# Kernel optimization log

Measured on AMD Instinct MI355X. Metric: run time of the kernel, lower is better.

The kernel has to match this reference:

```python
import jax, jax.numpy as jnp
import numpy as np

N, E = 50000, 800000
IN, HID, H, C = 128, 64, 4, 2
NEG_SLOPE = 0.2


def _gat_layer(h, src, dst, W, al, ar, b, out_dim, residual, resW=None, act='elu'):
    # h: [N, in]; W: [H*out, in]; al/ar: [H, out]; b: [H*out]
    n = h.shape[0]
    feat = (h @ W.T).reshape(n, H, out_dim)            # [N, H, out]
    el = jnp.einsum('nho,ho->nh', feat, al)            # [N, H]
    er = jnp.einsum('nho,ho->nh', feat, ar)            # [N, H]
    e = jax.nn.leaky_relu(el[src] + er[dst], NEG_SLOPE)  # [E, H]
    # segment softmax over incoming edges of each dst node
    emax = jax.ops.segment_max(e, dst, num_segments=n)
    ee = jnp.exp(e - emax[dst])
    denom = jax.ops.segment_sum(ee, dst, num_segments=n)
    alpha = ee / denom[dst]                             # [E, H]
    msg = feat[src] * alpha[:, :, None]                 # [E, H, out]
    rst = jax.ops.segment_sum(msg, dst, num_segments=n)  # [N, H, out]
    if residual == 'id':
        rst = rst + h.reshape(n, H, out_dim)
    elif residual == 'fc':
        rst = rst + (h @ resW.T).reshape(n, H, out_dim)
    rst = rst + b.reshape(1, H, out_dim)
    if act == 'elu':
        rst = jax.nn.elu(rst)
    else:  # softmax over last dim (F.softmax)
        rst = jax.nn.softmax(rst, axis=-1)
    return rst


def setup_inputs() -> dict:
    key = jax.random.key(0)
    ks = jax.random.split(key, 24)
    x = jax.random.normal(ks[0], (N, IN), dtype=jnp.float32)
    src = jax.random.randint(ks[1], (E,), 0, N)
    dst = jax.random.randint(ks[2], (E,), 0, N)
    s = 0.1
    d = {'x': x, 'src': src, 'dst': dst}
    # layer 1: IN -> (H, HID), no residual
    d['W1'] = jax.random.normal(ks[3], (H * HID, IN), dtype=jnp.float32) * s
    d['al1'] = jax.random.normal(ks[4], (H, HID), dtype=jnp.float32) * s
    d['ar1'] = jax.random.normal(ks[5], (H, HID), dtype=jnp.float32) * s
    d['b1'] = jnp.zeros((H * HID,), dtype=jnp.float32)
    # layers 2,3: H*HID -> (H, HID), identity residual
    d['W2'] = jax.random.normal(ks[6], (H * HID, H * HID), dtype=jnp.float32) * s
    d['al2'] = jax.random.normal(ks[7], (H, HID), dtype=jnp.float32) * s
    d['ar2'] = jax.random.normal(ks[8], (H, HID), dtype=jnp.float32) * s
    d['b2'] = jnp.zeros((H * HID,), dtype=jnp.float32)
    d['W3'] = jax.random.normal(ks[9], (H * HID, H * HID), dtype=jnp.float32) * s
    d['al3'] = jax.random.normal(ks[10], (H, HID), dtype=jnp.float32) * s
    d['ar3'] = jax.random.normal(ks[11], (H, HID), dtype=jnp.float32) * s
    d['b3'] = jnp.zeros((H * HID,), dtype=jnp.float32)
    # layer 4: H*HID -> (H, C), linear residual, softmax activation, mean over heads
    d['W4'] = jax.random.normal(ks[12], (H * C, H * HID), dtype=jnp.float32) * s
    d['al4'] = jax.random.normal(ks[13], (H, C), dtype=jnp.float32) * s
    d['ar4'] = jax.random.normal(ks[14], (H, C), dtype=jnp.float32) * s
    d['b4'] = jnp.zeros((H * C,), dtype=jnp.float32)
    d['resW4'] = jax.random.normal(ks[15], (H * C, H * HID), dtype=jnp.float32) * s
    return d


def reference(x, src, dst, W1, al1, ar1, b1, W2, al2, ar2, b2, W3, al3, ar3, b3, W4, al4, ar4, b4, resW4):
    h = _gat_layer(x, src, dst, W1, al1, ar1, b1, HID, 'none', act='elu').reshape(N, H * HID)
    h = _gat_layer(h, src, dst, W2, al2, ar2, b2, HID, 'id', act='elu').reshape(N, H * HID)
    h = _gat_layer(h, src, dst, W3, al3, ar3, b3, HID, 'id', act='elu').reshape(N, H * HID)
    h = _gat_layer(h, src, dst, W4, al4, ar4, b4, C, 'fc', resW=resW4, act='softmax')
    return h.mean(axis=1)  # [N, C]
```

## Files before the change

kernel.cpp:

```cpp
#include <hip/hip_runtime.h>
#include <hip/hip_bf16.h>
#include <math.h>


#define LEAKY_SLOPE 0.2f

typedef __bf16 bf16x8_t __attribute__((ext_vector_type(8)));
typedef float f32x4_t __attribute__((ext_vector_type(4)));
typedef float f32x2_t __attribute__((ext_vector_type(2)));

__device__ __forceinline__ float leaky(float x) { return x > 0.f ? x : LEAKY_SLOPE * x; }
__device__ __forceinline__ float eluf(float x)  { return x > 0.f ? x : expm1f(x); }
__device__ __forceinline__ float bflo(unsigned u) { return __uint_as_float(u << 16); }
__device__ __forceinline__ float bfhi(unsigned u) { return __uint_as_float(u & 0xffff0000u); }
__device__ __forceinline__ unsigned pk2(float a, float b) {
  __hip_bfloat162 t;
  t.x = __float2bfloat16(a);
  t.y = __float2bfloat16(b);
  return *(unsigned*)&t;
}

__device__ __forceinline__ float rlf(float v, int l) {
  return __uint_as_float((unsigned)__builtin_amdgcn_readlane((int)__float_as_uint(v), l));
}
template <int CTRL>
__device__ __forceinline__ float dpp_add(float x) {
  int t = __builtin_amdgcn_update_dpp(0, (int)__float_as_uint(x), CTRL, 0xf, 0xf, false);
  return x + __uint_as_float((unsigned)t);
}
__device__ __forceinline__ float wsum_dpp(float x) {
  x = dpp_add<0x111>(x);
  x = dpp_add<0x112>(x);
  x = dpp_add<0x114>(x);
  x = dpp_add<0x118>(x);
  x = dpp_add<0x142>(x);
  x = dpp_add<0x143>(x);
  return rlf(x, 63);
}
__device__ __forceinline__ float rowsum_dpp(float x) {
  x = dpp_add<0x111>(x);
  x = dpp_add<0x112>(x);
  x = dpp_add<0x114>(x);
  x = dpp_add<0x118>(x);
  return x;
}
__device__ __forceinline__ float wmax(float v) {
#pragma unroll
  for (int o = 32; o; o >>= 1) v = fmaxf(v, __shfl_xor(v, o));
  return v;
}
__device__ __forceinline__ float wsum_sh(float v) {
#pragma unroll
  for (int o = 32; o; o >>= 1) v += __shfl_xor(v, o);
  return v;
}

__device__ __forceinline__ void quad_fma(f32x2_t& a0, f32x2_t& a1, f32x2_t& a2, f32x2_t& a3,
                                         uint4 u, float w) {
  f32x2_t wv = {w, w};
  f32x2_t f;
  f[0] = bflo(u.x); f[1] = bfhi(u.x); a0 = __builtin_elementwise_fma(wv, f, a0);
  f[0] = bflo(u.y); f[1] = bfhi(u.y); a1 = __builtin_elementwise_fma(wv, f, a1);
  f[0] = bflo(u.z); f[1] = bfhi(u.z); a2 = __builtin_elementwise_fma(wv, f, a2);
  f[0] = bflo(u.w); f[1] = bfhi(u.w); a3 = __builtin_elementwise_fma(wv, f, a3);
}

__device__ __forceinline__ void gl_lds16(const __hip_bfloat16* g, __bf16* l) {
  __builtin_amdgcn_global_load_lds((const __attribute__((address_space(1))) void*)g,
                                   (__attribute__((address_space(3))) void*)l, 16, 0, 0);
}

__global__ __launch_bounds__(1024) void scan1_k(const int* __restrict__ deg,
                                                int* __restrict__ rowp,
                                                int* __restrict__ bsum, int n) {
  __shared__ int wtot[16];
  __shared__ int wpre[16];
  int tid = threadIdx.x, lane = tid & 63, wid = tid >> 6;
  int i = blockIdx.x * 1024 + tid;
  int v = (i < n) ? deg[i] : 0;
  int x = v;
#pragma unroll
  for (int off = 1; off < 64; off <<= 1) {
    int t = __shfl_up(x, off);
    if (lane >= off) x += t;
  }
  if (lane == 63) wtot[wid] = x;
  __syncthreads();
  if (wid == 0 && lane < 16) {
    int s = wtot[lane];
    int y = s;
#pragma unroll
    for (int off = 1; off < 16; off <<= 1) {
      int t = __shfl_up(y, off);
      if (lane >= off) y += t;
    }
    wpre[lane] = y - s;
    if (lane == 15) bsum[blockIdx.x] = y;
  }
  __syncthreads();
  if (i < n) rowp[i] = wpre[wid] + x - v;
}

__global__ void scan23_k(const int* __restrict__ bsum, int* __restrict__ rowp, int n, int nb) {
  __shared__ int pref[65];
  int tid = threadIdx.x;
  if (tid < 64) {
    int v = (tid < nb) ? bsum[tid] : 0;
    int x = v;
#pragma unroll
    for (int off = 1; off < 64; off <<= 1) {
      int t = __shfl_up(x, off);
      if (tid >= off) x += t;
    }
    pref[tid] = x - v;
    if (tid == 63) pref[64] = x;
  }
  __syncthreads();
  int i = blockIdx.x * 256 + tid;
  if (i < n) rowp[i] += pref[i >> 10];
  if (i == n) rowp[n] = pref[64];
}

__global__ void scatter_k(const int* __restrict__ src, const int* __restrict__ dst,
                          const int* __restrict__ rowp, const int* __restrict__ slot,
                          int* __restrict__ csrc, int e) {
  int i = blockIdx.x * 256 + threadIdx.x;
  if (i < e) csrc[rowp[dst[i]] + slot[i]] = src[i];
}

__global__ void cvthist_k(const float* __restrict__ W1, const float* __restrict__ W2,
                          const float* __restrict__ W3, const float* __restrict__ W4,
                          const float* __restrict__ rW4,
                          __hip_bfloat16* __restrict__ W1b, __hip_bfloat16* __restrict__ W2b,
                          __hip_bfloat16* __restrict__ W3b, __hip_bfloat16* __restrict__ Wcatb,
                          const int* __restrict__ dst, int* __restrict__ deg,
                          int* __restrict__ slot, int e) {
  int i = blockIdx.x * 256 + threadIdx.x;
  if (i < e) {
    int p = atomicAdd(&deg[dst[i]], 1);
    slot[i] = p;
  }
  if (i < 41984) {
    const float* sp;
    __hip_bfloat16* dp;
    int idx;
    if (i < 8192)       { sp = W1;  dp = W1b;          idx = i; }
    else if (i < 24576) { sp = W2;  dp = W2b;          idx = i - 8192; }
    else if (i < 40960) { sp = W3;  dp = W3b;          idx = i - 24576; }
    else if (i < 41472) { sp = W4;  dp = Wcatb;        idx = i - 40960; }
    else                { sp = rW4; dp = Wcatb + 2048; idx = i - 41472; }
    float4 wv = ((const float4*)sp)[idx];
    uint2 o = {pk2(wv.x, wv.y), pk2(wv.z, wv.w)};
    ((uint2*)dp)[idx] = o;
  }
}

__global__ __launch_bounds__(256) void gemm1f_mfma(const float* __restrict__ A,
                                                   const __hip_bfloat16* __restrict__ B,
                                                   __hip_bfloat16* __restrict__ featb,
                                                   const float* __restrict__ al,
                                                   const float* __restrict__ ar,
                                                   float* __restrict__ el,
                                                   float* __restrict__ er, int n, int nbx) {
  __shared__ __bf16 As[2][128 * 32];
  __shared__ __bf16 Bs[2][128 * 32];
  const int wg = blockIdx.x;
  const int b = ((wg >> 4) << 3) + (wg & 7);
  if (b >= nbx) return;
  const int cb = (wg >> 3) & 1;
  const int r0 = b * 128, c0 = cb * 128;

  const int tid = threadIdx.x;
  const int lane = tid & 63, w = tid >> 6;
  const int tm = lane & 15, tq = lane >> 4;
  const int wm = (w & 1) * 64, wn = (w >> 1) * 64;

  f32x4_t acc[4][4];
#pragma unroll
  for (int i = 0; i < 4; ++i)
#pragma unroll
    for (int j = 0; j < 4; ++j) acc[i][j] = 0.f;

  const int srow = tid >> 1;
  const int sh = tid & 1;
  const int arw = r0 + srow;
  const bool aok = arw < n;
  const float* ap = A + (size_t)arw * 128 + sh * 32;

  const int srB = w * 32 + (lane >> 2);
  const int scB = (lane & 3) * 8;
  const __hip_bfloat16* gb0 = B + (size_t)(c0 + srB) * 128 + scB;

#pragma unroll
  for (int kk = 0; kk < 128; kk += 64) {
    float4 av0 = {0, 0, 0, 0}, av1 = {0, 0, 0, 0}, av2 = {0, 0, 0, 0}, av3 = {0, 0, 0, 0};
    float4 av4 = {0, 0, 0, 0}, av5 = {0, 0, 0, 0}, av6 = {0, 0, 0, 0}, av7 = {0, 0, 0, 0};
    if (aok) {
      const float4* p = (const float4*)(ap + kk);
      av0 = p[0]; av1 = p[1]; av2 = p[2]; av3 = p[3];
      av4 = p[4]; av5 = p[5]; av6 = p[6]; av7 = p[7];
    }
    __syncthreads();
    const __hip_bfloat16* gbk = gb0 + kk;
    gl_lds16(gbk, &Bs[0][w * 1024]);
    gl_lds16(gbk + (size_t)16 * 128, &Bs[0][w * 1024 + 512]);
    gl_lds16(gbk + 32, &Bs[1][w * 1024]);
    gl_lds16(gbk + (size_t)16 * 128 + 32, &Bs[1][w * 1024 + 512]);
    {
      uint4 o;
      o.x = pk2(av0.x, av0.y); o.y = pk2(av0.z, av0.w);
      o.z = pk2(av1.x, av1.y); o.w = pk2(av1.z, av1.w);
      *(uint4*)&As[sh][srow * 32 + 0] = o;
      o.x = pk2(av2.x, av2.y); o.y = pk2(av2.z, av2.w);
      o.z = pk2(av3.x, av3.y); o.w = pk2(av3.z, av3.w);
      *(uint4*)&As[sh][srow * 32 + 8] = o;
      o.x = pk2(av4.x, av4.y); o.y = pk2(av4.z, av4.w);
      o.z = pk2(av5.x, av5.y); o.w = pk2(av5.z, av5.w);
      *(uint4*)&As[sh][srow * 32 + 16] = o;
      o.x = pk2(av6.x, av6.y); o.y = pk2(av6.z, av6.w);
      o.z = pk2(av7.x, av7.y); o.w = pk2(av7.z, av7.w);
      *(uint4*)&As[sh][srow * 32 + 24] = o;
    }
    __syncthreads();
#pragma unroll
    for (int ks = 0; ks < 2; ++ks) {
      bf16x8_t af[4], bfr[4];
#pragma unroll
      for (int i = 0; i < 4; ++i)
        af[i] = *(const bf16x8_t*)&As[ks][(wm + i * 16 + tm) * 32 + tq * 8];
#pragma unroll
      for (int j = 0; j < 4; ++j)
        bfr[j] = *(const bf16x8_t*)&Bs[ks][(wn + j * 16 + tm) * 32 + tq * 8];
#pragma unroll
      for (int i = 0; i < 4; ++i)
#pragma unroll
        for (int j = 0; j < 4; ++j)
          acc[i][j] = __builtin_amdgcn_mfma_f32_16x16x32_bf16(af[i], bfr[j], acc[i][j], 0, 0, 0);
    }
  }

#pragma unroll
  for (int i = 0; i < 4; ++i) {
#pragma unroll
    for (int j = 0; j < 4; ++j) {
      int col = c0 + wn + j * 16 + tm;
#pragma unroll
      for (int rr = 0; rr < 4; ++rr) {
        int row = r0 + wm + i * 16 + tq * 4 + rr;
        if (row < n) featb[(size_t)row * 256 + col] = __float2bfloat16(acc[i][j][rr]);
      }
    }
  }

  {
    const int hd = (c0 + wn) >> 6;
    float alv[4], arv[4];
#pragma unroll
    for (int j = 0; j < 4; ++j) {
      alv[j] = al[hd * 64 + j * 16 + tm];
      arv[j] = ar[hd * 64 + j * 16 + tm];
    }
#pragma unroll
    for (int i = 0; i < 4; ++i) {
#pragma unroll
      for (int rr = 0; rr < 4; ++rr) {
        float se = acc[i][0][rr] * alv[0] + acc[i][1][rr] * alv[1] +
                   acc[i][2][rr] * alv[2] + acc[i][3][rr] * alv[3];
        float sr2 = acc[i][0][rr] * arv[0] + acc[i][1][rr] * arv[1] +
                    acc[i][2][rr] * arv[2] + acc[i][3][rr] * arv[3];
        se = rowsum_dpp(se);
        sr2 = rowsum_dpp(sr2);
        if (tm == 15) {
          int row = r0 + wm + i * 16 + tq * 4 + rr;
          if (row < n) {
            el[(size_t)row * 4 + hd] = se;
            er[(size_t)row * 4 + hd] = sr2;
          }
        }
      }
    }
  }
}

template <int K>
__global__ __launch_bounds__(256) void gemm_mfma(const __hip_bfloat16* __restrict__ A,
                                                 const __hip_bfloat16* __restrict__ B,
                                                 __hip_bfloat16* __restrict__ featb,
                                                 const float* __restrict__ al,
                                                 const float* __restrict__ ar,
                                                 float* __restrict__ el,
                                                 float* __restrict__ er, int n, int nbx) {
  __shared__ __bf16 As[2][128 * 32];
  __shared__ __bf16 Bs[2][128 * 32];
  const int wg = blockIdx.x;
  const int b = ((wg >> 4) << 3) + (wg & 7);
  if (b >= nbx) return;
  const int cb = (wg >> 3) & 1;
  const int r0 = b * 128, c0 = cb * 128;

  const int tid = threadIdx.x;
  const int lane = tid & 63, w = tid >> 6;
  const int tm = lane & 15, tq = lane >> 4;
  const int wm = (w & 1) * 64, wn = (w >> 1) * 64;

  f32x4_t acc[4][4];
#pragma unroll
  for (int i = 0; i < 4; ++i)
#pragma unroll
    for (int j = 0; j < 4; ++j) acc[i][j] = 0.f;

  const bool interior = (r0 + 128 <= n);
  if (interior) {
    const int srow = w * 32 + (lane >> 2);
    const int scol = (lane & 3) * 8;
    const __hip_bfloat16* ga0 = A + (size_t)(r0 + srow) * K + scol;
    const __hip_bfloat16* gb0 = B + (size_t)(c0 + srow) * K + scol;
    for (int kk = 0; kk < K; kk += 64) {
      const __hip_bfloat16* ga = ga0 + kk;
      const __hip_bfloat16* gb = gb0 + kk;
      __syncthreads();
      gl_lds16(ga, &As[0][w * 1024]);
      gl_lds16(ga + (size_t)16 * K, &As[0][w * 1024 + 512]);
      gl_lds16(ga + 32, &As[1][w * 1024]);
      gl_lds16(ga + (size_t)16 * K + 32, &As[1][w * 1024 + 512]);
      gl_lds16(gb, &Bs[0][w * 1024]);
      gl_lds16(gb + (size_t)16 * K, &Bs[0][w * 1024 + 512]);
      gl_lds16(gb + 32, &Bs[1][w * 1024]);
      gl_lds16(gb + (size_t)16 * K + 32, &Bs[1][w * 1024 + 512]);
      __syncthreads();
#pragma unroll
      for (int ks = 0; ks < 2; ++ks) {
        bf16x8_t af[4], bfr[4];
#pragma unroll
        for (int i = 0; i < 4; ++i)
          af[i] = *(const bf16x8_t*)&As[ks][(wm + i * 16 + tm) * 32 + tq * 8];
#pragma unroll
        for (int j = 0; j < 4; ++j)
          bfr[j] = *(const bf16x8_t*)&Bs[ks][(wn + j * 16 + tm) * 32 + tq * 8];
#pragma unroll
        for (int i = 0; i < 4; ++i)
#pragma unroll
          for (int j = 0; j < 4; ++j)
            acc[i][j] = __builtin_amdgcn_mfma_f32_16x16x32_bf16(af[i], bfr[j], acc[i][j], 0, 0, 0);
      }
    }
  } else {
    const int srow = tid >> 1, sko = (tid & 1) * 16;
    for (int kk = 0; kk < K; kk += 32) {
      uint4 av0 = {0, 0, 0, 0}, av1 = {0, 0, 0, 0};
      int arw = r0 + srow;
      if (arw < n) {
        const uint4* p = (const uint4*)(A + (size_t)arw * K + kk + sko);
        av0 = p[0];
        av1 = p[1];
      }
      const uint4* q = (const uint4*)(B + (size_t)(c0 + srow) * K + kk + sko);
      uint4 bv0 = q[0], bv1 = q[1];
      __syncthreads();
      *(uint4*)&As[0][srow * 32 + sko] = av0;
      *(uint4*)&As[0][srow * 32 + sko + 8] = av1;
      *(uint4*)&Bs[0][srow * 32 + sko] = bv0;
      *(uint4*)&Bs[0][srow * 32 + sko + 8] = bv1;
      __syncthreads();
      bf16x8_t af[4], bfr[4];
#pragma unroll
      for (int i = 0; i < 4; ++i)
        af[i] = *(const bf16x8_t*)&As[0][(wm + i * 16 + tm) * 32 + tq * 8];
#pragma unroll
      for (int j = 0; j < 4; ++j)
        bfr[j] = *(const bf16x8_t*)&Bs[0][(wn + j * 16 + tm) * 32 + tq * 8];
#pragma unroll
      for (int i = 0; i < 4; ++i)
#pragma unroll
        for (int j = 0; j < 4; ++j)
          acc[i][j] = __builtin_amdgcn_mfma_f32_16x16x32_bf16(af[i], bfr[j], acc[i][j], 0, 0, 0);
    }
  }

#pragma unroll
  for (int i = 0; i < 4; ++i) {
#pragma unroll
    for (int j = 0; j < 4; ++j) {
      int col = c0 + wn + j * 16 + tm;
#pragma unroll
      for (int rr = 0; rr < 4; ++rr) {
        int row = r0 + wm + i * 16 + tq * 4 + rr;
        if (row < n) featb[(size_t)row * 256 + col] = __float2bfloat16(acc[i][j][rr]);
      }
    }
  }

  {
    const int hd = (c0 + wn) >> 6;
    float alv[4], arv[4];
#pragma unroll
    for (int j = 0; j < 4; ++j) {
      alv[j] = al[hd * 64 + j * 16 + tm];
      arv[j] = ar[hd * 64 + j * 16 + tm];
    }
#pragma unroll
    for (int i = 0; i < 4; ++i) {
#pragma unroll
      for (int rr = 0; rr < 4; ++rr) {
        float se = acc[i][0][rr] * alv[0] + acc[i][1][rr] * alv[1] +
                   acc[i][2][rr] * alv[2] + acc[i][3][rr] * alv[3];
        float sr2 = acc[i][0][rr] * arv[0] + acc[i][1][rr] * arv[1] +
                    acc[i][2][rr] * arv[2] + acc[i][3][rr] * arv[3];
        se = rowsum_dpp(se);
        sr2 = rowsum_dpp(sr2);
        if (tm == 15) {
          int row = r0 + wm + i * 16 + tq * 4 + rr;
          if (row < n) {
            el[(size_t)row * 4 + hd] = se;
            er[(size_t)row * 4 + hd] = sr2;
          }
        }
      }
    }
  }
}

template <int RES>
__global__ __launch_bounds__(256) void agg64_k(const __hip_bfloat16* __restrict__ featb,
                                               const float* __restrict__ el,
                                               const float* __restrict__ er,
                                               const int* __restrict__ rowp,
                                               const int* __restrict__ csrc,
                                               const __hip_bfloat16* __restrict__ hinb,
                                               const float* __restrict__ bias,
                                               __hip_bfloat16* __restrict__ houtb, int n) {
  __shared__ float wsh[4][256];
  __shared__ int ssh[4][64];
  int wv = threadIdx.x >> 6;
  int node = blockIdx.x * 4 + wv;
  int lane = threadIdx.x & 63;
  if (node >= n) return;
  int s0 = rowp[node], s1 = rowp[node + 1];
  int deg = s1 - s0;
  float4 erv = *(const float4*)(er + (size_t)node * 4);

  if (deg <= 64) {
    int sown = 0;
    float x0 = 0.f, x1 = 0.f, x2 = 0.f, x3 = 0.f;
    if (lane < deg) {
      sown = csrc[s0 + lane];
      float4 e = *(const float4*)(el + (size_t)sown * 4);
      x0 = __expf(leaky(e.x + erv.x));
      x1 = __expf(leaky(e.y + erv.y));
      x2 = __expf(leaky(e.z + erv.z));
      x3 = __expf(leaky(e.w + erv.w));
    }
    float d0 = wsum_dpp(x0), d1 = wsum_dpp(x1), d2 = wsum_dpp(x2), d3 = wsum_dpp(x3);
    float i0 = d0 > 0.f ? 1.f / d0 : 0.f;
    float i1 = d1 > 0.f ? 1.f / d1 : 0.f;
    float i2 = d2 > 0.f ? 1.f / d2 : 0.f;
    float i3 = d3 > 0.f ? 1.f / d3 : 0.f;
    float4 wq = {x0 * i0, x1 * i1, x2 * i2, x3 * i3};
    *(float4*)&wsh[wv][lane * 4] = wq;
    ssh[wv][lane] = sown;

    const int half = lane >> 5, sub = lane & 31;
    const int hh = sub >> 3;
    f32x2_t a0 = {0.f, 0.f}, a1 = {0.f, 0.f}, a2 = {0.f, 0.f}, a3 = {0.f, 0.f};
    const int G = deg >> 3;
    int k = 0;
    if (G) {
      int ke = half;
      int sk0 = ssh[wv][ke], sk1 = ssh[wv][ke + 2];
      int sk2 = ssh[wv][ke + 4], sk3 = ssh[wv][ke + 6];
      uint4 u0 = ((const uint4*)(featb + ((size_t)sk0 << 8)))[sub];
      uint4 u1 = ((const uint4*)(featb + ((size_t)sk1 << 8)))[sub];
      uint4 u2 = ((const uint4*)(featb + ((size_t)sk2 << 8)))[sub];
      uint4 u3 = ((const uint4*)(featb + ((size_t)sk3 << 8)))[sub];
      float w0 = wsh[wv][ke * 4 + hh];
      float w1 = wsh[wv][(ke + 2) * 4 + hh];
      float w2 = wsh[wv][(ke + 4) * 4 + hh];
      float w3 = wsh[wv][(ke + 6) * 4 + hh];
      for (int g = 1; g < G; ++g) {
        int kb = g * 8 + half;
        int t0 = ssh[wv][kb], t1 = ssh[wv][kb + 2];
        int t2 = ssh[wv][kb + 4], t3 = ssh[wv][kb + 6];
        uint4 v0 = ((const uint4*)(featb + ((size_t)t0 << 8)))[sub];
        uint4 v1 = ((const uint4*)(featb + ((size_t)t1 << 8)))[sub];
        uint4 v2 = ((const uint4*)(featb + ((size_t)t2 << 8)))[sub];
        uint4 v3 = ((const uint4*)(featb + ((size_t)t3 << 8)))[sub];
        float y0 = wsh[wv][kb * 4 + hh];
        float y1 = wsh[wv][(kb + 2) * 4 + hh];
        float y2 = wsh[wv][(kb + 4) * 4 + hh];
        float y3 = wsh[wv][(kb + 6) * 4 + hh];
        quad_fma(a0, a1, a2, a3, u0, w0);
        quad_fma(a0, a1, a2, a3, u1, w1);
        quad_fma(a0, a1, a2, a3, u2, w2);
        quad_fma(a0, a1, a2, a3, u3, w3);
        u0 = v0; u1 = v1; u2 = v2; u3 = v3;
        w0 = y0; w1 = y1; w2 = y2; w3 = y3;
      }
      quad_fma(a0, a1, a2, a3, u0, w0);
      quad_fma(a0, a1, a2, a3, u1, w1);
      quad_fma(a0, a1, a2, a3, u2, w2);
      quad_fma(a0, a1, a2, a3, u3, w3);
      k = G * 8;
    }
    for (; k < deg; k += 2) {
      int ke = k + half;
      int sk = ssh[wv][ke];
      uint4 u = ((const uint4*)(featb + ((size_t)sk << 8)))[sub];
      float wk = wsh[wv][ke * 4 + hh];
      quad_fma(a0, a1, a2, a3, u, wk);
    }
    a0[0] += __shfl_xor(a0[0], 32); a0[1] += __shfl_xor(a0[1], 32);
    a1[0] += __shfl_xor(a1[0], 32); a1[1] += __shfl_xor(a1[1], 32);
    a2[0] += __shfl_xor(a2[0], 32); a2[1] += __shfl_xor(a2[1], 32);
    a3[0] += __shfl_xor(a3[0], 32); a3[1] += __shfl_xor(a3[1], 32);

    if (half == 0) {
      size_t base = (size_t)node * 256 + sub * 8;
      float v0 = a0[0], v1 = a0[1], v2 = a1[0], v3 = a1[1];
      float v4 = a2[0], v5 = a2[1], v6 = a3[0], v7 = a3[1];
      float4 b0 = *(const float4*)(bias + sub * 8);
      float4 b1 = *(const float4*)(bias + sub * 8 + 4);
      v0 += b0.x; v1 += b0.y; v2 += b0.z; v3 += b0.w;
      v4 += b1.x; v5 += b1.y; v6 += b1.z; v7 += b1.w;
      if (RES) {
        uint4 r = *(const uint4*)(hinb + base);
        v0 += bflo(r.x); v1 += bfhi(r.x);
        v2 += bflo(r.y); v3 += bfhi(r.y);
        v4 += bflo(r.z); v5 += bfhi(r.z);
        v6 += bflo(r.w); v7 += bfhi(r.w);
      }
      uint4 o;
      o.x = pk2(eluf(v0), eluf(v1));
      o.y = pk2(eluf(v2), eluf(v3));
      o.z = pk2(eluf(v4), eluf(v5));
      o.w = pk2(eluf(v6), eluf(v7));
      *(uint4*)(houtb + base) = o;
    }
  } else {
    int hsel = lane >> 4;
    f32x2_t a01 = {0.f, 0.f}, a23 = {0.f, 0.f};
    float m0 = -INFINITY, m1 = -INFINITY, m2 = -INFINITY, m3 = -INFINITY;
    for (int k = s0 + lane; k < s1; k += 64) {
      int s = csrc[k];
      float4 e = *(const float4*)(el + (size_t)s * 4);
      m0 = fmaxf(m0, leaky(e.x + erv.x));
      m1 = fmaxf(m1, leaky(e.y + erv.y));
      m2 = fmaxf(m2, leaky(e.z + erv.z));
      m3 = fmaxf(m3, leaky(e.w + erv.w));
    }
    m0 = wmax(m0); m1 = wmax(m1); m2 = wmax(m2); m3 = wmax(m3);
    float d0 = 0, d1 = 0, d2 = 0, d3 = 0;
    for (int k = s0 + lane; k < s1; k += 64) {
      int s = csrc[k];
      float4 e = *(const float4*)(el + (size_t)s * 4);
      d0 += __expf(leaky(e.x + erv.x) - m0);
      d1 += __expf(leaky(e.y + erv.y) - m1);
      d2 += __expf(leaky(e.z + erv.z) - m2);
      d3 += __expf(leaky(e.w + erv.w) - m3);
    }
    d0 = wsum_sh(d0); d1 = wsum_sh(d1); d2 = wsum_sh(d2); d3 = wsum_sh(d3);
    float j0 = d0 > 0.f ? 1.f / d0 : 0.f;
    float j1 = d1 > 0.f ? 1.f / d1 : 0.f;
    float j2 = d2 > 0.f ? 1.f / d2 : 0.f;
    float j3 = d3 > 0.f ? 1.f / d3 : 0.f;
    for (int k = s0; k < s1; ++k) {
      int s = csrc[k];
      float4 e = *(const float4*)(el + (size_t)s * 4);
      float w0 = __expf(leaky(e.x + erv.x) - m0) * j0;
      float w1 = __expf(leaky(e.y + erv.y) - m1) * j1;
      float w2 = __expf(leaky(e.z + erv.z) - m2) * j2;
      float w3 = __expf(leaky(e.w + erv.w) - m3) * j3;
      float wk = (hsel == 0) ? w0 : (hsel == 1) ? w1 : (hsel == 2) ? w2 : w3;
      uint2 u = ((const uint2*)(featb + ((size_t)s << 8)))[lane];
      f32x2_t wv2 = {wk, wk};
      f32x2_t f;
      f[0] = bflo(u.x); f[1] = bfhi(u.x); a01 = __builtin_elementwise_fma(wv2, f, a01);
      f[0] = bflo(u.y); f[1] = bfhi(u.y); a23 = __builtin_elementwise_fma(wv2, f, a23);
    }
    size_t base = (size_t)node * 256 + lane * 4;
    float4 bv = *(const float4*)(bias + lane * 4);
    float v0 = a01[0] + bv.x, v1 = a01[1] + bv.y;
    float v2 = a23[0] + bv.z, v3 = a23[1] + bv.w;
    if (RES) {
      uint2 r = *(const uint2*)(hinb + base);
      v0 += bflo(r.x); v1 += bfhi(r.x);
      v2 += bflo(r.y); v3 += bfhi(r.y);
    }
    uint2 o;
    o.x = pk2(eluf(v0), eluf(v1));
    o.y = pk2(eluf(v2), eluf(v3));
    *(uint2*)(houtb + base) = o;
  }
}

__global__ __launch_bounds__(256) void l4mfma_k(const __hip_bfloat16* __restrict__ hb,
                                                const __hip_bfloat16* __restrict__ Wcat,
                                                const float* __restrict__ al4,
                                                const float* __restrict__ ar4,
                                                float* __restrict__ feat4,
                                                float* __restrict__ res4,
                                                float* __restrict__ el4,
                                                float* __restrict__ er4, int n) {
  int wid = blockIdx.x * 4 + (threadIdx.x >> 6);
  int n16 = (n + 15) >> 4;
  if (wid >= n16) return;
  int lane = threadIdx.x & 63;
  int tm = lane & 15, tq = lane >> 4;
  int row = wid * 16 + tm;
  int rowc = row < n ? row : n - 1;
  const __hip_bfloat16* ap = hb + (size_t)rowc * 256 + tq * 8;
  const __hip_bfloat16* bp = Wcat + (size_t)tm * 256 + tq * 8;
  f32x4_t acc = {0.f, 0.f, 0.f, 0.f};
#pragma unroll
  for (int k = 0; k < 8; ++k) {
    bf16x8_t af = *(const bf16x8_t*)(ap + k * 32);
    bf16x8_t bf = *(const bf16x8_t*)(bp + k * 32);
    acc = __builtin_amdgcn_mfma_f32_16x16x32_bf16(af, bf, acc, 0, 0, 0);
  }
  float* dstp = (tm < 8) ? feat4 : res4;
  int cc = tm & 7;
  float a4 = (tm < 8) ? al4[tm] : 0.f;
  float r4 = (tm < 8) ? ar4[tm] : 0.f;
#pragma unroll
  for (int r = 0; r < 4; ++r) {
    int node = wid * 16 + tq * 4 + r;
    float te = acc[r] * a4;
    float tr = acc[r] * r4;
    te += __shfl_xor(te, 1);
    tr += __shfl_xor(tr, 1);
    if (node < n) {
      dstp[(size_t)node * 8 + cc] = acc[r];
      if (tm < 8 && (tm & 1) == 0) {
        el4[(size_t)node * 4 + (tm >> 1)] = te;
        er4[(size_t)node * 4 + (tm >> 1)] = tr;
      }
    }
  }
}

__global__ __launch_bounds__(256) void agg4_k(const float* __restrict__ feat4,
                                              const float* __restrict__ el4,
                                              const float* __restrict__ er4,
                                              const int* __restrict__ rowp,
                                              const int* __restrict__ csrc,
                                              const float* __restrict__ res4,
                                              const float* __restrict__ b4,
                                              float* __restrict__ out, int n) {
  int wv = threadIdx.x >> 6;
  int node = blockIdx.x * 4 + wv;
  int lane = threadIdx.x & 63;
  if (node >= n) return;
  int s0 = rowp[node], s1 = rowp[node + 1];
  int deg = s1 - s0;
  float4 erv = *(const float4*)(er4 + (size_t)node * 4);
  float v = 0.f;

  if (deg <= 64) {
    int sown = 0;
    float x0 = 0.f, x1 = 0.f, x2 = 0.f, x3 = 0.f;
    if (lane < deg) {
      sown = csrc[s0 + lane];
      float4 e = *(const float4*)(el4 + (size_t)sown * 4);
      x0 = __expf(leaky(e.x + erv.x));
      x1 = __expf(leaky(e.y + erv.y));
      x2 = __expf(leaky(e.z + erv.z));
      x3 = __expf(leaky(e.w + erv.w));
    }
    float d0 = wsum_dpp(x0), d1 = wsum_dpp(x1), d2 = wsum_dpp(x2), d3 = wsum_dpp(x3);
    float w0 = x0 * (d0 > 0.f ? 1.f / d0 : 0.f);
    float w1 = x1 * (d1 > 0.f ? 1.f / d1 : 0.f);
    float w2 = x2 * (d2 > 0.f ? 1.f / d2 : 0.f);
    float w3 = x3 * (d3 > 0.f ? 1.f / d3 : 0.f);
    float4 f0 = {0, 0, 0, 0}, f1 = {0, 0, 0, 0};
    if (lane < deg) {
      const float4* fp = (const float4*)(feat4 + (size_t)sown * 8);
      f0 = fp[0];
      f1 = fp[1];
    }
    float t0 = w0 * f0.x, t1 = w0 * f0.y;
    float t2 = w1 * f0.z, t3 = w1 * f0.w;
    float t4 = w2 * f1.x, t5 = w2 * f1.y;
    float t6 = w3 * f1.z, t7 = w3 * f1.w;
    t0 = wsum_dpp(t0); t1 = wsum_dpp(t1); t2 = wsum_dpp(t2); t3 = wsum_dpp(t3);
    t4 = wsum_dpp(t4); t5 = wsum_dpp(t5); t6 = wsum_dpp(t6); t7 = wsum_dpp(t7);
    int p = lane & 7;
    float s = t0;
    s = (p == 1) ? t1 : s; s = (p == 2) ? t2 : s; s = (p == 3) ? t3 : s;
    s = (p == 4) ? t4 : s; s = (p == 5) ? t5 : s; s = (p == 6) ? t6 : s;
    s = (p == 7) ? t7 : s;
    if (lane < 8) v = s + res4[(size_t)node * 8 + lane] + b4[lane];
  } else {
    int p = lane & 7, hh = p >> 1;
    float acc = 0.f;
    float m0 = -INFINITY, m1 = -INFINITY, m2 = -INFINITY, m3 = -INFINITY;
    for (int k = s0 + lane; k < s1; k += 64) {
      int s = csrc[k];
      float4 e = *(const float4*)(el4 + (size_t)s * 4);
      m0 = fmaxf(m0, leaky(e.x + erv.x));
      m1 = fmaxf(m1, leaky(e.y + erv.y));
      m2 = fmaxf(m2, leaky(e.z + erv.z));
      m3 = fmaxf(m3, leaky(e.w + erv.w));
    }
    m0 = wmax(m0); m1 = wmax(m1); m2 = wmax(m2); m3 = wmax(m3);
    float d0 = 0, d1 = 0, d2 = 0, d3 = 0;
    for (int k = s0 + lane; k < s1; k += 64) {
      int s = csrc[k];
      float4 e = *(const float4*)(el4 + (size_t)s * 4);
      d0 += __expf(leaky(e.x + erv.x) - m0);
      d1 += __expf(leaky(e.y + erv.y) - m1);
      d2 += __expf(leaky(e.z + erv.z) - m2);
      d3 += __expf(leaky(e.w + erv.w) - m3);
    }
    d0 = wsum_sh(d0); d1 = wsum_sh(d1); d2 = wsum_sh(d2); d3 = wsum_sh(d3);
    float i0 = d0 > 0.f ? 1.f / d0 : 0.f;
    float i1 = d1 > 0.f ? 1.f / d1 : 0.f;
    float i2 = d2 > 0.f ? 1.f / d2 : 0.f;
    float i3 = d3 > 0.f ? 1.f / d3 : 0.f;
    for (int k = s0; k < s1; ++k) {
      int s = csrc[k];
      float4 e = *(const float4*)(el4 + (size_t)s * 4);
      float w0 = __expf(leaky(e.x + erv.x) - m0) * i0;
      float w1 = __expf(leaky(e.y + erv.y) - m1) * i1;
      float w2 = __expf(leaky(e.z + erv.z) - m2) * i2;
      float w3 = __expf(leaky(e.w + erv.w) - m3) * i3;
      float wk = (hh == 0) ? w0 : (hh == 1) ? w1 : (hh == 2) ? w2 : w3;
      if (lane < 8) acc = fmaf(wk, feat4[(size_t)s * 8 + p], acc);
    }
    if (lane < 8) v = acc + res4[(size_t)node * 8 + lane] + b4[lane];
  }

  float pv = __shfl_xor(v, 1);
  float mx = fmaxf(v, pv);
  float ex = __expf(v - mx);
  float sm = ex + __shfl_xor(ex, 1);
  float pr = ex / sm;
  float t = pr + __shfl_xor(pr, 2);
  t += __shfl_xor(t, 4);
  if (lane < 2) out[(size_t)node * 2 + lane] = t * 0.25f;
}

extern "C" void kernel_launch(void* const* d_in, const int* in_sizes, int n_in,
                              void* d_out, int out_size, void* d_ws, size_t ws_size,
                              hipStream_t stream) {
  const float* x   = (const float*)d_in[0];
  const int* src   = (const int*)d_in[1];
  const int* dst   = (const int*)d_in[2];
  const float* W1  = (const float*)d_in[3];
  const float* al1 = (const float*)d_in[4];
  const float* ar1 = (const float*)d_in[5];
  const float* b1  = (const float*)d_in[6];
  const float* W2  = (const float*)d_in[7];
  const float* al2 = (const float*)d_in[8];
  const float* ar2 = (const float*)d_in[9];
  const float* b2  = (const float*)d_in[10];
  const float* W3  = (const float*)d_in[11];
  const float* al3 = (const float*)d_in[12];
  const float* ar3 = (const float*)d_in[13];
  const float* b3  = (const float*)d_in[14];
  const float* W4  = (const float*)d_in[15];
  const float* al4 = (const float*)d_in[16];
  const float* ar4 = (const float*)d_in[17];
  const float* b4  = (const float*)d_in[18];
  const float* rW4 = (const float*)d_in[19];
  float* out = (float*)d_out;

  const int n = in_sizes[0] / 128;
  const int e = in_sizes[1];

  char* ws = (char*)d_ws;
  auto alloc = [&](size_t bytes) -> char* {
    char* p = ws;
    ws += (bytes + 255) & ~(size_t)255;
    return p;
  };
  __hip_bfloat16* featb = (__hip_bfloat16*)alloc((size_t)n * 256 * 2);
  __hip_bfloat16* h1b   = (__hip_bfloat16*)alloc((size_t)n * 256 * 2);
  __hip_bfloat16* h2b   = (__hip_bfloat16*)alloc((size_t)n * 256 * 2);
  __hip_bfloat16* h3b   = (__hip_bfloat16*)alloc((size_t)n * 256 * 2);
  __hip_bfloat16* W1b   = (__hip_bfloat16*)alloc((size_t)256 * 128 * 2);
  __hip_bfloat16* W2b   = (__hip_bfloat16*)alloc((size_t)256 * 256 * 2);
  __hip_bfloat16* W3b   = (__hip_bfloat16*)alloc((size_t)256 * 256 * 2);
  __hip_bfloat16* Wcatb = (__hip_bfloat16*)alloc((size_t)16 * 256 * 2);
  float* el    = (float*)alloc((size_t)n * 4 * 4);
  float* er    = (float*)alloc((size_t)n * 4 * 4);
  float* feat4 = (float*)alloc((size_t)n * 8 * 4);
  float* res4  = (float*)alloc((size_t)n * 8 * 4);
  float* el4   = (float*)alloc((size_t)n * 4 * 4);
  float* er4   = (float*)alloc((size_t)n * 4 * 4);
  int* deg     = (int*)alloc((size_t)n * 4);
  int* rowp    = (int*)alloc((size_t)(n + 1) * 4);
  int* csrc    = (int*)alloc((size_t)e * 4);
  int* slot    = (int*)alloc((size_t)e * 4);
  int nb_scan  = (n + 1023) / 1024;
  int* bsum    = (int*)alloc((size_t)(nb_scan + 1) * 4);

  (void)hipMemsetAsync(deg, 0, (size_t)n * 4, stream);

  cvthist_k<<<(e + 255) / 256, 256, 0, stream>>>(W1, W2, W3, W4, rW4, W1b, W2b, W3b,
                                                 Wcatb, dst, deg, slot, e);
  scan1_k<<<nb_scan, 1024, 0, stream>>>(deg, rowp, bsum, n);
  scan23_k<<<(n + 256) / 256, 256, 0, stream>>>(bsum, rowp, n, nb_scan);
  scatter_k<<<(e + 255) / 256, 256, 0, stream>>>(src, dst, rowp, slot, csrc, e);

  int nbx = (n + 127) / 128;
  int ggx = ((2 * nbx + 15) / 16) * 16;
  int nb4 = (n + 3) / 4;

  gemm1f_mfma<<<ggx, 256, 0, stream>>>(x, W1b, featb, al1, ar1, el, er, n, nbx);
  agg64_k<0><<<nb4, 256, 0, stream>>>(featb, el, er, rowp, csrc, nullptr, b1, h1b, n);
  gemm_mfma<256><<<ggx, 256, 0, stream>>>(h1b, W2b, featb, al2, ar2, el, er, n, nbx);
  agg64_k<1><<<nb4, 256, 0, stream>>>(featb, el, er, rowp, csrc, h1b, b2, h2b, n);
  gemm_mfma<256><<<ggx, 256, 0, stream>>>(h2b, W3b, featb, al3, ar3, el, er, n, nbx);
  agg64_k<1><<<nb4, 256, 0, stream>>>(featb, el, er, rowp, csrc, h2b, b3, h3b, n);
  int n16 = (n + 15) / 16;
  l4mfma_k<<<(n16 + 3) / 4, 256, 0, stream>>>(h3b, Wcatb, al4, ar4, feat4, res4, el4, er4, n);
  agg4_k<<<nb4, 256, 0, stream>>>(feat4, el4, er4, rowp, csrc, res4, b4, out, n);
}
```

Baseline: 449.6 us.

## Fuse CSR build into one persistent kernel with software grid barriers

Replaces the memset, histogram/convert, two scan kernels and scatter kernel with a single 512-block persistent kernel that uses atomic-counter grid barriers between phases. The scan now processes 4 elements per thread in 256-thread blocks, and the final offsets are written to a separate rowpf array. This is meant to remove several kernel-launch gaps and tail effects in the graph preprocessing. It relies on all 512 blocks being co-resident, otherwise the spin barriers can deadlock, and it adds barrier spin overhead.

```diff
diff --git a/kernel.cpp b/kernel.cpp
--- a/kernel.cpp
+++ b/kernel.cpp
@@ -70,77 +70,37 @@
                                    (__attribute__((address_space(3))) void*)l, 16, 0, 0);
 }
 
-__global__ __launch_bounds__(1024) void scan1_k(const int* __restrict__ deg,
-                                                int* __restrict__ rowp,
-                                                int* __restrict__ bsum, int n) {
-  __shared__ int wtot[16];
-  __shared__ int wpre[16];
-  int tid = threadIdx.x, lane = tid & 63, wid = tid >> 6;
-  int i = blockIdx.x * 1024 + tid;
-  int v = (i < n) ? deg[i] : 0;
-  int x = v;
-#pragma unroll
-  for (int off = 1; off < 64; off <<= 1) {
-    int t = __shfl_up(x, off);
-    if (lane >= off) x += t;
-  }
-  if (lane == 63) wtot[wid] = x;
+__device__ __forceinline__ void gsync(int* bar, int target) {
   __syncthreads();
-  if (wid == 0 && lane < 16) {
-    int s = wtot[lane];
-    int y = s;
-#pragma unroll
-    for (int off = 1; off < 16; off <<= 1) {
-      int t = __shfl_up(y, off);
-      if (lane >= off) y += t;
-    }
-    wpre[lane] = y - s;
-    if (lane == 15) bsum[blockIdx.x] = y;
+  __threadfence();
+  if (threadIdx.x == 0) {
+    atomicAdd(bar, 1);
+    while (__hip_atomic_load(bar, __ATOMIC_RELAXED, __HIP_MEMORY_SCOPE_AGENT) < target)
+      __builtin_amdgcn_s_sleep(8);
   }
   __syncthreads();
-  if (i < n) rowp[i] = wpre[wid] + x - v;
-}
-
-__global__ void scan23_k(const int* __restrict__ bsum, int* __restrict__ rowp, int n, int nb) {
-  __shared__ int pref[65];
-  int tid = threadIdx.x;
-  if (tid < 64) {
-    int v = (tid < nb) ? bsum[tid] : 0;
-    int x = v;
-#pragma unroll
-    for (int off = 1; off < 64; off <<= 1) {
-      int t = __shfl_up(x, off);
-      if (tid >= off) x += t;
-    }
-    pref[tid] = x - v;
-    if (tid == 63) pref[64] = x;
-  }
-  __syncthreads();
-  int i = blockIdx.x * 256 + tid;
-  if (i < n) rowp[i] += pref[i >> 10];
-  if (i == n) rowp[n] = pref[64];
-}
-
-__global__ void scatter_k(const int* __restrict__ src, const int* __restrict__ dst,
-                          const int* __restrict__ rowp, const int* __restrict__ slot,
-                          int* __restrict__ csrc, int e) {
-  int i = blockIdx.x * 256 + threadIdx.x;
-  if (i < e) csrc[rowp[dst[i]] + slot[i]] = src[i];
-}
-
-__global__ void cvthist_k(const float* __restrict__ W1, const float* __restrict__ W2,
-                          const float* __restrict__ W3, const float* __restrict__ W4,
-                          const float* __restrict__ rW4,
-                          __hip_bfloat16* __restrict__ W1b, __hip_bfloat16* __restrict__ W2b,
-                          __hip_bfloat16* __restrict__ W3b, __hip_bfloat16* __restrict__ Wcatb,
-                          const int* __restrict__ dst, int* __restrict__ deg,
-                          int* __restrict__ slot, int e) {
-  int i = blockIdx.x * 256 + threadIdx.x;
-  if (i < e) {
-    int p = atomicAdd(&deg[dst[i]], 1);
-    slot[i] = p;
-  }
-  if (i < 41984) {
+  __threadfence();
+}
+
+__global__ __launch_bounds__(256) void csr_k(
+    const float* __restrict__ W1, const float* __restrict__ W2,
+    const float* __restrict__ W3, const float* __restrict__ W4,
+    const float* __restrict__ rW4,
+    __hip_bfloat16* __restrict__ W1b, __hip_bfloat16* __restrict__ W2b,
+    __hip_bfloat16* __restrict__ W3b, __hip_bfloat16* __restrict__ Wcatb,
+    const int* __restrict__ src, const int* __restrict__ dst,
+    int* __restrict__ deg, int* __restrict__ slot,
+    int* __restrict__ rowp, int* __restrict__ rowpf,
+    int* __restrict__ bsum, int* __restrict__ bpre,
+    int* __restrict__ csrc, int* __restrict__ bar,
+    int n, int e) {
+  const int tid = threadIdx.x, bid = blockIdx.x;
+  const int gsz = gridDim.x * 256;
+  const int gi = bid * 256 + tid;
+  const int nch = (n + 1023) >> 10;
+
+  for (int i = gi; i < n; i += gsz) deg[i] = 0;
+  for (int i = gi; i < 41984; i += gsz) {
     const float* sp;
     __hip_bfloat16* dp;
     int idx;
@@ -153,6 +113,74 @@
     uint2 o = {pk2(wv.x, wv.y), pk2(wv.z, wv.w)};
     ((uint2*)dp)[idx] = o;
   }
+  gsync(bar, gridDim.x * 1);
+
+  for (int i = gi; i < e; i += gsz) slot[i] = atomicAdd(&deg[dst[i]], 1);
+  gsync(bar, gridDim.x * 2);
+
+  __shared__ int wtot[4], wpre[4];
+  if (bid < nch) {
+    int base = bid << 10;
+    int idx = base + tid * 4;
+    int d0 = 0, d1 = 0, d2 = 0, d3 = 0;
+    if (idx + 3 < n) {
+      int4 q = *(const int4*)(deg + idx);
+      d0 = q.x; d1 = q.y; d2 = q.z; d3 = q.w;
+    } else {
+      if (idx < n)     d0 = deg[idx];
+      if (idx + 1 < n) d1 = deg[idx + 1];
+      if (idx + 2 < n) d2 = deg[idx + 2];
+      if (idx + 3 < n) d3 = deg[idx + 3];
+    }
+    int t = d0 + d1 + d2 + d3;
+    int lane = tid & 63, wv2 = tid >> 6;
+    int X = t;
+#pragma unroll
+    for (int off = 1; off < 64; off <<= 1) {
+      int u = __shfl_up(X, off);
+      if (lane >= off) X += u;
+    }
+    if (lane == 63) wtot[wv2] = X;
+    __syncthreads();
+    if (tid < 4) {
+      int s4 = wtot[tid];
+      int y = s4;
+#pragma unroll
+      for (int off = 1; off < 4; off <<= 1) {
+        int u = __shfl_up(y, off);
+        if (tid >= off) y += u;
+      }
+      wpre[tid] = y - s4;
+      if (tid == 3) bsum[bid] = y;
+    }
+    __syncthreads();
+    int ex = wpre[wv2] + X - t;
+    if (idx < n)     rowp[idx]     = ex;
+    if (idx + 1 < n) rowp[idx + 1] = ex + d0;
+    if (idx + 2 < n) rowp[idx + 2] = ex + d0 + d1;
+    if (idx + 3 < n) rowp[idx + 3] = ex + d0 + d1 + d2;
+  }
+  gsync(bar, gridDim.x * 3);
+
+  if (bid == 0 && tid < 64) {
+    int v = (tid < nch) ? bsum[tid] : 0;
+    int x = v;
+#pragma unroll
+    for (int off = 1; off < 64; off <<= 1) {
+      int u = __shfl_up(x, off);
+      if (tid >= off) x += u;
+    }
+    if (tid < nch) bpre[tid] = x - v;
+    if (tid == nch - 1) bpre[nch] = x;
+  }
+  gsync(bar, gridDim.x * 4);
+
+  for (int i = gi; i < e; i += gsz) {
+    int d = dst[i];
+    csrc[rowp[d] + bpre[d >> 10] + slot[i]] = src[i];
+  }
+  for (int i = gi; i <= n; i += gsz)
+    rowpf[i] = (i == n) ? bpre[nch] : rowp[i] + bpre[i >> 10];
 }
 
 __global__ __launch_bounds__(256) void gemm1f_mfma(const float* __restrict__ A,
@@ -788,30 +816,30 @@
   float* er4   = (float*)alloc((size_t)n * 4 * 4);
   int* deg     = (int*)alloc((size_t)n * 4);
   int* rowp    = (int*)alloc((size_t)(n + 1) * 4);
+  int* rowpf   = (int*)alloc((size_t)(n + 1) * 4);
   int* csrc    = (int*)alloc((size_t)e * 4);
   int* slot    = (int*)alloc((size_t)e * 4);
-  int nb_scan  = (n + 1023) / 1024;
-  int* bsum    = (int*)alloc((size_t)(nb_scan + 1) * 4);
-
-  (void)hipMemsetAsync(deg, 0, (size_t)n * 4, stream);
-
-  cvthist_k<<<(e + 255) / 256, 256, 0, stream>>>(W1, W2, W3, W4, rW4, W1b, W2b, W3b,
-                                                 Wcatb, dst, deg, slot, e);
-  scan1_k<<<nb_scan, 1024, 0, stream>>>(deg, rowp, bsum, n);
-  scan23_k<<<(n + 256) / 256, 256, 0, stream>>>(bsum, rowp, n, nb_scan);
-  scatter_k<<<(e + 255) / 256, 256, 0, stream>>>(src, dst, rowp, slot, csrc, e);
+  int* bsum    = (int*)alloc((size_t)64 * 4);
+  int* bpre    = (int*)alloc((size_t)66 * 4);
+  int* bar     = (int*)alloc((size_t)64 * 4);
+
+  (void)hipMemsetAsync(bar, 0, 4, stream);
+
+  csr_k<<<512, 256, 0, stream>>>(W1, W2, W3, W4, rW4, W1b, W2b, W3b, Wcatb,
+                                 src, dst, deg, slot, rowp, rowpf, bsum, bpre,
+                                 csrc, bar, n, e);
 
   int nbx = (n + 127) / 128;
   int ggx = ((2 * nbx + 15) / 16) * 16;
   int nb4 = (n + 3) / 4;
 
   gemm1f_mfma<<<ggx, 256, 0, stream>>>(x, W1b, featb, al1, ar1, el, er, n, nbx);
-  agg64_k<0><<<nb4, 256, 0, stream>>>(featb, el, er, rowp, csrc, nullptr, b1, h1b, n);
+  agg64_k<0><<<nb4, 256, 0, stream>>>(featb, el, er, rowpf, csrc, nullptr, b1, h1b, n);
   gemm_mfma<256><<<ggx, 256, 0, stream>>>(h1b, W2b, featb, al2, ar2, el, er, n, nbx);
-  agg64_k<1><<<nb4, 256, 0, stream>>>(featb, el, er, rowp, csrc, h1b, b2, h2b, n);
+  agg64_k<1><<<nb4, 256, 0, stream>>>(featb, el, er, rowpf, csrc, h1b, b2, h2b, n);
   gemm_mfma<256><<<ggx, 256, 0, stream>>>(h2b, W3b, featb, al3, ar3, el, er, n, nbx);
-  agg64_k<1><<<nb4, 256, 0, stream>>>(featb, el, er, rowp, csrc, h2b, b3, h3b, n);
+  agg64_k<1><<<nb4, 256, 0, stream>>>(featb, el, er, rowpf, csrc, h2b, b3, h3b, n);
   int n16 = (n + 15) / 16;
   l4mfma_k<<<(n16 + 3) / 4, 256, 0, stream>>>(h3b, Wcatb, al4, ar4, feat4, res4, el4, er4, n);
-  agg4_k<<<nb4, 256, 0, stream>>>(feat4, el4, er4, rowp, csrc, res4, b4, out, n);
-}
+  agg4_k<<<nb4, 256, 0, stream>>>(feat4, el4, er4, rowpf, csrc, res4, b4, out, n);
+}
```

Result: slower. 772.7 us (+71.9%).
